# Optimization experiments

Measured on AMD Instinct MI355X. Metric: run time of the kernel, lower is better.

## Reference

```python
import jax, jax.numpy as jnp
import numpy as np

HIDDEN = 1024
Q_OUT = 2048
KV_OUT = 1024
HEAD_DIM = 128
N_Q = Q_OUT // HEAD_DIM      # 16
N_KV = KV_OUT // HEAD_DIM    # 8
EPS = 1e-6
ROPE_BASE = 10000.0


def _rms_norm(x, w, eps=EPS):
    # normalize over last dim (head_dim)
    ms = jnp.mean(x * x, axis=-1, keepdims=True)
    return x * jax.lax.rsqrt(ms + eps) * w


def _rope_cos_sin(t, dim=HEAD_DIM, base=ROPE_BASE):
    inv_freq = 1.0 / (base ** (jnp.arange(0, dim, 2, dtype=jnp.float32) / dim))
    pos = jnp.arange(t, dtype=jnp.float32)
    freqs = pos[:, None] * inv_freq[None, :]          # (T, D/2)
    emb = jnp.concatenate([freqs, freqs], axis=-1)    # (T, D)
    return jnp.cos(emb), jnp.sin(emb)


def _rotate_half(x):
    d = x.shape[-1] // 2
    return jnp.concatenate([-x[..., d:], x[..., :d]], axis=-1)


def setup_inputs() -> dict:
    key = jax.random.key(0)
    ks = jax.random.split(key, 7)
    def lin(k, fan_in, fan_out):
        # nn.Linear default init: U(-1/sqrt(fan_in), 1/sqrt(fan_in)); stored as (in, out) for x @ W
        bound = 1.0 / np.sqrt(fan_in)
        return jax.random.uniform(k, (fan_in, fan_out), jnp.float32, -bound, bound)
    return {
        "x": jax.random.normal(ks[0], (2, 2048, HIDDEN), jnp.float32),
        "Wq": lin(ks[1], HIDDEN, Q_OUT),
        "Wk": lin(ks[2], HIDDEN, KV_OUT),
        "Wv": lin(ks[3], HIDDEN, KV_OUT),
        "Wo": lin(ks[4], Q_OUT, HIDDEN),
        "q_norm_w": jnp.ones((HEAD_DIM,), jnp.float32),
        "k_norm_w": jnp.ones((HEAD_DIM,), jnp.float32),
    }


def reference(x, Wq, Wk, Wv, Wo, q_norm_w, k_norm_w):
    b, t, _ = x.shape
    # QKV projections, shaped to (B, H, T, D)
    q = (x @ Wq).reshape(b, t, N_Q, HEAD_DIM).transpose(0, 2, 1, 3)
    k = (x @ Wk).reshape(b, t, N_KV, HEAD_DIM).transpose(0, 2, 1, 3)
    v = (x @ Wv).reshape(b, t, N_KV, HEAD_DIM).transpose(0, 2, 1, 3)
    # per-head RMSNorm on q/k
    q = _rms_norm(q, q_norm_w)
    k = _rms_norm(k, k_norm_w)
    # RoPE (positions 0..T-1)
    cos, sin = _rope_cos_sin(t)                        # (T, D)
    cos = cos[None, None]; sin = sin[None, None]       # (1,1,T,D)
    q = q * cos + _rotate_half(q) * sin
    k = k * cos + _rotate_half(k) * sin
    # GQA: repeat_interleave kv heads to match q heads
    rep = N_Q // N_KV
    k_r = jnp.repeat(k, rep, axis=1)                   # (B, Hq, T, D)
    v_r = jnp.repeat(v, rep, axis=1)
    # causal attention
    scores = jnp.einsum('bhqd,bhkd->bhqk', q, k_r) / jnp.sqrt(jnp.asarray(HEAD_DIM, x.dtype))
    causal = jnp.triu(jnp.full((t, t), -jnp.inf, dtype=scores.dtype), k=1)[None, None]
    attn = jax.nn.softmax(scores + causal, axis=-1)
    out = jnp.einsum('bhqk,bhkd->bhqd', attn, v_r)     # (B, Hq, T, D)
    out = out.transpose(0, 2, 1, 3).reshape(b, t, Q_OUT)
    return out @ Wo
```

## Files before the change

kernel.cpp:

```cpp
#include <hip/hip_runtime.h>
#include <math.h>

typedef __attribute__((ext_vector_type(8))) short short8;
typedef __attribute__((ext_vector_type(4))) float f32x4;
typedef __attribute__((ext_vector_type(4))) unsigned int uint4v;

#define HIDDEN 1024
#define QOUT 2048
#define KVOUT 1024
#define HD 128
#define TSEQ 2048

__device__ __forceinline__ float bf2f(unsigned short h) {
    union { unsigned int u; float f; } x; x.u = ((unsigned int)h) << 16; return x.f;
}
__device__ __forceinline__ unsigned short f2bf(float f) {
    union { float f; unsigned int u; } x; x.f = f;
    unsigned int r = (x.u + 0x7fffu + ((x.u >> 16) & 1u)) >> 16;
    return (unsigned short)r;
}
__device__ __forceinline__ unsigned int cvtpk(float lo, float hi) {
    unsigned int r;
    asm("v_cvt_pk_bf16_f32 %0, %1, %2" : "=v"(r) : "v"(lo), "v"(hi));
    return r;
}

__device__ __forceinline__ void glds16(const unsigned short* g, unsigned short* l) {
    __builtin_amdgcn_global_load_lds(
        (const __attribute__((address_space(1))) unsigned int*)g,
        (__attribute__((address_space(3))) unsigned int*)l, 16, 0, 0);
}

__global__ __launch_bounds__(256) void prep(const float* __restrict__ x,
                                            const float* __restrict__ Wq,
                                            const float* __restrict__ Wk,
                                            const float* __restrict__ Wv,
                                            const float* __restrict__ Wo,
                                            unsigned short* __restrict__ xb,
                                            unsigned short* __restrict__ Wt,
                                            unsigned short* __restrict__ Wot) {
    int bid = blockIdx.x;
    int tid = threadIdx.x;
    if (bid < 4096) {
        int i = bid * 256 + tid;
        float4 v = *(const float4*)(x + (size_t)i * 4);
        unsigned short o[4] = {f2bf(v.x), f2bf(v.y), f2bf(v.z), f2bf(v.w)};
        *(unsigned long long*)(xb + (size_t)i * 4) = *(unsigned long long*)o;
        return;
    }
    bid -= 4096;
    const float* W; unsigned short* D; int K, N;
    if (bid < 512)       { W = Wq; D = Wt;                          K = 1024; N = 2048; }
    else if (bid < 768)  { bid -= 512;  W = Wk; D = Wt + (size_t)2048 * 1024; K = 1024; N = 1024; }
    else if (bid < 1024) { bid -= 768;  W = Wv; D = Wt + (size_t)3072 * 1024; K = 1024; N = 1024; }
    else                 { bid -= 1024; W = Wo; D = Wot;                      K = 2048; N = 1024; }
    __shared__ __attribute__((aligned(16))) unsigned short Ls[64 * 72];
    int ntiles = N >> 6;
    int kt = bid / ntiles, nt = bid - kt * ntiles;
    int k0 = kt * 64, n0 = nt * 64;
    for (int t = 0; t < 4; t++) {
        int idx = tid + t * 256;
        int r = idx >> 4, seg = idx & 15;
        float4 v = *(const float4*)(W + (size_t)(k0 + r) * N + n0 + seg * 4);
        int c = seg * 4;
        Ls[(c + 0) * 72 + r] = f2bf(v.x);
        Ls[(c + 1) * 72 + r] = f2bf(v.y);
        Ls[(c + 2) * 72 + r] = f2bf(v.z);
        Ls[(c + 3) * 72 + r] = f2bf(v.w);
    }
    __syncthreads();
    for (int t = 0; t < 2; t++) {
        int idx = tid + t * 256;
        int rr = idx >> 3, seg = idx & 7;
        uint4v v = *(const uint4v*)(Ls + rr * 72 + seg * 8);
        *(uint4v*)(D + (size_t)(n0 + rr) * K + k0 + seg * 8) = v;
    }
}

template <int OUT_BF16>
__global__ __launch_bounds__(256) void gemm_o(const unsigned short* __restrict__ A,
                                              const unsigned short* __restrict__ Bt,
                                              void* __restrict__ Cout,
                                              int M, int N, int K) {
    __shared__ __attribute__((aligned(16))) unsigned short As[2][128 * 64];
    __shared__ __attribute__((aligned(16))) unsigned short Bs[2][64 * 64];
    const int tid = threadIdx.x;
    const int lane = tid & 63;
    const int warp = tid >> 6;
    const int ln = lane & 15;
    const int quad = lane >> 4;
    const int m0 = blockIdx.y * 128;
    const int n0 = blockIdx.x * 64;

    const int srow = lane >> 3;
    const int schunk = (lane & 7) ^ srow;
    const unsigned short* Ag = A + (size_t)(m0 + warp * 32 + srow) * K + schunk * 8;
    const unsigned short* Bg = Bt + (size_t)(n0 + warp * 16 + srow) * K + schunk * 8;

    f32x4 acc[2][4];
#pragma unroll
    for (int i = 0; i < 2; i++)
#pragma unroll
        for (int j = 0; j < 4; j++) acc[i][j] = (f32x4){0.f, 0.f, 0.f, 0.f};

    auto stage = [&](int k0, int bi) {
#pragma unroll
        for (int g = 0; g < 4; g++)
            glds16(Ag + (size_t)(g * 8) * K + k0, As[bi] + (warp * 32 + g * 8) * 64);
#pragma unroll
        for (int g = 0; g < 2; g++)
            glds16(Bg + (size_t)(g * 8) * K + k0, Bs[bi] + (warp * 16 + g * 8) * 64);
    };

    const int KI = K >> 6;
    stage(0, 0);
    for (int it = 0; it < KI; it++) {
        __syncthreads();
        if (it + 1 < KI) stage((it + 1) << 6, (it + 1) & 1);
        const unsigned short* Ab = As[it & 1];
        const unsigned short* Bb = Bs[it & 1];
#pragma unroll
        for (int ks = 0; ks < 2; ks++) {
            const int rc = ((ks << 2) + quad) ^ (ln & 7);
            short8 af[2], bf[4];
#pragma unroll
            for (int mt = 0; mt < 2; mt++)
                af[mt] = *(const short8*)(Ab + (warp * 32 + mt * 16 + ln) * 64 + rc * 8);
#pragma unroll
            for (int nt = 0; nt < 4; nt++)
                bf[nt] = *(const short8*)(Bb + (nt * 16 + ln) * 64 + rc * 8);
#pragma unroll
            for (int mt = 0; mt < 2; mt++)
#pragma unroll
                for (int nt = 0; nt < 4; nt++)
                    acc[mt][nt] = __builtin_amdgcn_mfma_f32_16x16x32_bf16(bf[nt], af[mt], acc[mt][nt], 0, 0, 0);
        }
    }
#pragma unroll
    for (int mt = 0; mt < 2; mt++) {
        int row = m0 + warp * 32 + mt * 16 + ln;
#pragma unroll
        for (int nt = 0; nt < 4; nt++) {
            int colb = n0 + nt * 16 + quad * 4;
            if (OUT_BF16) {
                unsigned long long pk =
                    (unsigned long long)cvtpk(acc[mt][nt][0], acc[mt][nt][1]) |
                    ((unsigned long long)cvtpk(acc[mt][nt][2], acc[mt][nt][3]) << 32);
                *(unsigned long long*)((unsigned short*)Cout + (size_t)row * N + colb) = pk;
            } else {
                *(f32x4*)((float*)Cout + (size_t)row * N + colb) = acc[mt][nt];
            }
        }
    }
}

__global__ __launch_bounds__(256) void nrvt(const unsigned short* __restrict__ QKV,
                                            const float* __restrict__ qw,
                                            const float* __restrict__ kw,
                                            unsigned short* __restrict__ Q,
                                            unsigned short* __restrict__ Kb,
                                            unsigned short* __restrict__ Vt) {
    if (blockIdx.x < 12288) {
        const int tid = threadIdx.x;
        const int l5 = tid & 31;
        const int task = blockIdx.x * 8 + (tid >> 5);
        const int tok = task / 24;
        const int slot = task - tok * 24;
        const int b = tok >> 11, t = tok & 2047;
        const float* w;
        unsigned short* dst;
        int col0;
        float sc;
        if (slot < 16) {
            col0 = slot * HD;
            dst = Q + ((size_t)(b * 16 + slot) * TSEQ + t) * HD;
            w = qw;
            sc = 0.12750580997495268f;
        } else {
            int hk = slot - 16;
            col0 = QOUT + hk * HD;
            dst = Kb + ((size_t)(b * 8 + hk) * TSEQ + t) * HD;
            w = kw;
            sc = 1.0f;
        }
        const unsigned short* row = QKV + (size_t)tok * 4096 + col0;
        unsigned long long pkin = *(const unsigned long long*)(row + l5 * 4);
        unsigned short us[4];
        *(unsigned long long*)us = pkin;
        float e[4];
        float ss = 0.f;
#pragma unroll
        for (int k = 0; k < 4; k++) { e[k] = bf2f(us[k]); ss += e[k] * e[k]; }
#pragma unroll
        for (int off = 1; off < 32; off <<= 1) ss += __shfl_xor(ss, off);
        float rr = rsqrtf(ss * (1.0f / 128.0f) + 1e-6f);
        float4 wv = *(const float4*)(w + l5 * 4);
        float n[4] = { e[0] * rr * wv.x, e[1] * rr * wv.y, e[2] * rr * wv.z, e[3] * rr * wv.w };
        float np[4];
#pragma unroll
        for (int k = 0; k < 4; k++) np[k] = __shfl_xor(n[k], 16);
        const float tf = (float)t;
        const int fb = (l5 & 15) * 4;
        const bool hi = (l5 >= 16);
        unsigned short outs[4];
#pragma unroll
        for (int k = 0; k < 4; k++) {
            float invf = __builtin_exp2f(-(float)(fb + k) * 0.20762050593045951f);
            float sf, cf;
            __sincosf(tf * invf, &sf, &cf);
            float o = hi ? (n[k] * cf + np[k] * sf) : (n[k] * cf - np[k] * sf);
            outs[k] = f2bf(o * sc);
        }
        *(unsigned long long*)(dst + l5 * 4) = *(unsigned long long*)outs;
        return;
    }
    __shared__ __attribute__((aligned(16))) unsigned short Ls[128 * 72];
    int bid = blockIdx.x - 12288;
    int tt = bid & 31, hk = (bid >> 5) & 7, b = bid >> 8;
    int t0 = tt * 64;
    int tid = threadIdx.x;
    const unsigned short* base = QKV + (size_t)(b * 2048 + t0) * 4096 + 3072 + hk * 128;
    for (int i = 0; i < 4; i++) {
        int idx = tid + i * 256;
        int r = idx >> 4, seg = idx & 15;
        uint4v v = *(const uint4v*)(base + (size_t)r * 4096 + seg * 8);
        unsigned short* pv = (unsigned short*)&v;
        int d = seg * 8;
        for (int jj = 0; jj < 8; jj++) Ls[(d + jj) * 72 + r] = pv[jj];
    }
    __syncthreads();
    unsigned short* out = Vt + (size_t)(b * 8 + hk) * 128 * 2048;
    for (int i = 0; i < 4; i++) {
        int idx = tid + i * 256;
        int d = idx >> 3, seg = idx & 7;
        uint4v v = *(const uint4v*)(Ls + d * 72 + seg * 8);
        *(uint4v*)(out + (size_t)d * 2048 + t0 + seg * 8) = v;
    }
}

__global__ __launch_bounds__(512, 4) void attn(const unsigned short* __restrict__ Q,
                                               const unsigned short* __restrict__ Kg,
                                               const unsigned short* __restrict__ Vt,
                                               unsigned short* __restrict__ Og) {
    __shared__ __attribute__((aligned(16))) unsigned short Ks[2][64 * 128];
    __shared__ __attribute__((aligned(16))) unsigned short Vs[2][128 * 64];
    __shared__ __attribute__((aligned(16))) unsigned short Ps[8][8][16][8];
    const int p = blockIdx.x;
    const int bh = blockIdx.y;
    const int b = bh >> 4, h = bh & 15, hk = h >> 1;
    const int tid = threadIdx.x;
    const int w = tid >> 6, lane = tid & 63, ln = lane & 15, quad = lane >> 4;
    const int sg = w >> 2;
    const int wi = w & 3;
    const int tile = sg ? (31 - p) : p;
    const int jdiag = tile;
    const int qrow0 = tile * 64 + wi * 16;

    const unsigned short* Kbase = Kg + (size_t)(b * 8 + hk) * TSEQ * HD;
    const unsigned short* Vbase = Vt + (size_t)(b * 8 + hk) * HD * TSEQ;
    const unsigned short* Qh = Q + (size_t)(b * 16 + h) * TSEQ * HD;

    short8 qf[4];
#pragma unroll
    for (int kt = 0; kt < 4; kt++)
        qf[kt] = *(const short8*)(Qh + (size_t)(qrow0 + ln) * HD + kt * 32 + quad * 8);

    f32x4 o[8];
    f32x4 lac = (f32x4){0.f, 0.f, 0.f, 0.f};
#pragma unroll
    for (int ot = 0; ot < 8; ot++) o[ot] = (f32x4){0.f, 0.f, 0.f, 0.f};
    float m_ = -1e30f;

    const int kr = lane >> 4;
    const int kc = lane & 15;
    const int vr = lane >> 3;
    const int vc = lane & 7;

    auto stage_kv = [&](int jt, int bi) {
        const int j0s = jt * 64;
        unsigned short* KsB = Ks[bi];
        unsigned short* VsB = Vs[bi];
#pragma unroll
        for (int c = 0; c < 2; c++) {
            int row = w * 8 + c * 4 + kr;
            glds16(Kbase + (size_t)(j0s + row) * HD + ((kc ^ (row & 15)) * 8),
                   KsB + (w * 8 + c * 4) * 128);
        }
#pragma unroll
        for (int c = 0; c < 2; c++) {
            int d = w * 16 + c * 8 + vr;
            glds16(Vbase + (size_t)d * TSEQ + j0s + ((vc ^ (d & 7)) * 8),
                   VsB + (w * 16 + c * 8) * 64);
        }
    };

    short8 ones8;
#pragma unroll
    for (int i = 0; i < 8; i++) ones8[i] = (short)0x3F80;

    unsigned short* Pw = &Ps[w][0][0][0];
    const int nT = 32 - p;
    stage_kv(0, 0);
    for (int j = 0; j < nT; j++) {
        __syncthreads();
        if (j + 1 < nT) stage_kv(j + 1, (j + 1) & 1);
        const unsigned short* KsC = Ks[j & 1];
        const unsigned short* VsC = Vs[j & 1];
        const bool act = sg ? true : (j <= jdiag);
        if (act) {
            f32x4 s[4];
#pragma unroll
            for (int kb = 0; kb < 4; kb++) s[kb] = (f32x4){0.f, 0.f, 0.f, 0.f};
            __builtin_amdgcn_s_setprio(1);
#pragma unroll
            for (int kt = 0; kt < 4; kt++) {
                short8 kf[4];
#pragma unroll
                for (int kb = 0; kb < 4; kb++)
                    kf[kb] = *(const short8*)(KsC + (kb * 16 + ln) * 128 + (((kt * 4 + quad) ^ ln) * 8));
#pragma unroll
                for (int kb = 0; kb < 4; kb++)
                    s[kb] = __builtin_amdgcn_mfma_f32_16x16x32_bf16(kf[kb], qf[kt], s[kb], 0, 0, 0);
            }
            __builtin_amdgcn_s_setprio(0);
            float mk[4];
            if (j == jdiag) {
                const int qloc = wi * 16 + ln;
#pragma unroll
                for (int kb = 0; kb < 4; kb++) {
#pragma unroll
                    for (int r = 0; r < 4; r++) {
                        int kvloc = kb * 16 + quad * 4 + r;
                        if (kvloc > qloc) s[kb][r] = -1e30f;
                    }
                    mk[kb] = fmaxf(fmaxf(s[kb][0], s[kb][1]), fmaxf(s[kb][2], s[kb][3]));
                }
            } else {
#pragma unroll
                for (int kb = 0; kb < 4; kb++)
                    mk[kb] = fmaxf(fmaxf(s[kb][0], s[kb][1]), fmaxf(s[kb][2], s[kb][3]));
            }
            float mx = fmaxf(fmaxf(mk[0], mk[1]), fmaxf(mk[2], mk[3]));
            float mn = m_;
            bool needR = false;
            float alpha = 1.f;
            if (!__all(mx <= mn + 8.0f)) {
                mx = fmaxf(mx, __shfl_xor(mx, 16));
                mx = fmaxf(mx, __shfl_xor(mx, 32));
                mn = fmaxf(m_, mx);
                alpha = __builtin_exp2f(m_ - mn);
                m_ = mn;
                needR = true;
            }
#pragma unroll
            for (int kb = 0; kb < 4; kb++) {
                float p0 = __builtin_exp2f(s[kb][0] - mn);
                float p1 = __builtin_exp2f(s[kb][1] - mn);
                float p2 = __builtin_exp2f(s[kb][2] - mn);
                float p3 = __builtin_exp2f(s[kb][3] - mn);
                unsigned long long pk =
                    (unsigned long long)cvtpk(p0, p1) |
                    ((unsigned long long)cvtpk(p2, p3) << 32);
                *(unsigned long long*)(Pw + (2 * kb + (quad >> 1)) * 128 + ln * 8 + (quad & 1) * 4) = pk;
            }
            short8 pf0 = *(const short8*)(Pw + quad * 128 + ln * 8);
            short8 pf1 = *(const short8*)(Pw + (4 + quad) * 128 + ln * 8);
            if (needR) {
#pragma unroll
                for (int ot = 0; ot < 8; ot++)
#pragma unroll
                    for (int r = 0; r < 4; r++) o[ot][r] *= alpha;
#pragma unroll
                for (int r = 0; r < 4; r++) lac[r] *= alpha;
            }
            __builtin_amdgcn_s_setprio(1);
            lac = __builtin_amdgcn_mfma_f32_16x16x32_bf16(ones8, pf0, lac, 0, 0, 0);
            lac = __builtin_amdgcn_mfma_f32_16x16x32_bf16(ones8, pf1, lac, 0, 0, 0);
#pragma unroll
            for (int ot = 0; ot < 8; ot++) {
                short8 vf0 = *(const short8*)(VsC + (ot * 16 + ln) * 64 + ((quad ^ (ln & 7)) * 8));
                short8 vf1 = *(const short8*)(VsC + (ot * 16 + ln) * 64 + (((4 + quad) ^ (ln & 7)) * 8));
                o[ot] = __builtin_amdgcn_mfma_f32_16x16x32_bf16(vf0, pf0, o[ot], 0, 0, 0);
                o[ot] = __builtin_amdgcn_mfma_f32_16x16x32_bf16(vf1, pf1, o[ot], 0, 0, 0);
            }
            __builtin_amdgcn_s_setprio(0);
        }
    }
    float inv = 1.0f / lac[0];
    size_t rowoff = ((size_t)(b * TSEQ + qrow0 + ln)) * QOUT + h * 128 + quad * 4;
#pragma unroll
    for (int ot = 0; ot < 8; ot++) {
        unsigned long long pk =
            (unsigned long long)cvtpk(o[ot][0] * inv, o[ot][1] * inv) |
            ((unsigned long long)cvtpk(o[ot][2] * inv, o[ot][3] * inv) << 32);
        *(unsigned long long*)(Og + rowoff + ot * 16) = pk;
    }
}

extern "C" void kernel_launch(void* const* d_in, const int* in_sizes, int n_in,
                              void* d_out, int out_size, void* d_ws, size_t ws_size,
                              hipStream_t stream) {
    (void)in_sizes; (void)n_in; (void)out_size;
    const float* x  = (const float*)d_in[0];
    const float* Wq = (const float*)d_in[1];
    const float* Wk = (const float*)d_in[2];
    const float* Wv = (const float*)d_in[3];
    const float* Wo = (const float*)d_in[4];
    const float* qw = (const float*)d_in[5];
    const float* kw = (const float*)d_in[6];

    char* ws = (char*)d_ws;
    const size_t MB = 1024 * 1024;
    unsigned short* Wt   = (unsigned short*)(ws);
    unsigned short* Wot  = (unsigned short*)(ws + 8 * MB);
    unsigned short* QKVb = (unsigned short*)(ws + 12 * MB);
    unsigned short* xb   = (unsigned short*)(ws + 44 * MB);
    unsigned short* Qb   = (unsigned short*)(ws + 52 * MB);
    unsigned short* Kb   = (unsigned short*)(ws + 68 * MB);
    unsigned short* Vtb  = (unsigned short*)(ws + 76 * MB);
    unsigned short* Ob   = (unsigned short*)(ws + 84 * MB);
    if (ws_size < 100 * MB) return;

    prep<<<dim3(5632), 256, 0, stream>>>(x, Wq, Wk, Wv, Wo, xb, Wt, Wot);
    gemm_o<1><<<dim3(64, 32), 256, 0, stream>>>(xb, Wt, QKVb, 4096, 4096, 1024);
    nrvt<<<dim3(12800), 256, 0, stream>>>(QKVb, qw, kw, Qb, Kb, Vtb);
    attn<<<dim3(16, 32), 512, 0, stream>>>(Qb, Kb, Vtb, Ob);
    gemm_o<0><<<dim3(16, 32), 256, 0, stream>>>(Ob, Wot, (float*)d_out, 4096, 1024, 2048);
}
```

Baseline: 254.4 us.

## Add 256x256 8-wave QKV GEMM, permlane P-repack, and balanced attention tile order

Replaces the QKV projection GEMM with a new 512-thread kernel using 256x256 tiles, a double-buffered LDS pipeline and interleaved barriers. The aim is more operand reuse and better overlap of global loads with MFMA work. In attention, the P matrix is now repacked into MFMA operand layout with permlane16/32 swaps instead of an LDS round trip. Causal tiles are also remapped so short and long blocks alternate. Together these target LDS traffic, GEMM memory bandwidth and load imbalance, at the cost of more registers and a more intricate fragment layout that must stay correct.

```diff
diff --git a/kernel.cpp b/kernel.cpp
--- a/kernel.cpp
+++ b/kernel.cpp
@@ -23,6 +23,12 @@
     unsigned int r;
     asm("v_cvt_pk_bf16_f32 %0, %1, %2" : "=v"(r) : "v"(lo), "v"(hi));
     return r;
+}
+__device__ __forceinline__ void pl32(unsigned int& a, unsigned int& b) {
+    asm("v_permlane32_swap_b32 %0, %1" : "+v"(a), "+v"(b));
+}
+__device__ __forceinline__ void pl16(unsigned int& a, unsigned int& b) {
+    asm("v_permlane16_swap_b32 %0, %1" : "+v"(a), "+v"(b));
 }
 
 __device__ __forceinline__ void glds16(const unsigned short* g, unsigned short* l) {
@@ -75,6 +81,140 @@
         uint4v v = *(const uint4v*)(Ls + rr * 72 + seg * 8);
         *(uint4v*)(D + (size_t)(n0 + rr) * K + k0 + seg * 8) = v;
     }
+}
+
+__global__ __launch_bounds__(512, 2) void gemm8(const unsigned short* __restrict__ A,
+                                                const unsigned short* __restrict__ Bt,
+                                                unsigned short* __restrict__ Cout,
+                                                int M, int N, int K) {
+    (void)M;
+    __shared__ __attribute__((aligned(16))) unsigned short L[2][4][128 * 64];
+    const int tid = threadIdx.x;
+    const int lane = tid & 63;
+    const int w = tid >> 6;
+    const int ln = lane & 15;
+    const int quad = lane >> 4;
+    const int wm2 = w >> 2;
+    const int wn4 = w & 3;
+    const int m0 = blockIdx.y * 256;
+    const int n0 = blockIdx.x * 256;
+
+    const int srow8 = lane >> 3;
+    const int schunk = (lane & 7) ^ srow8;
+    const int KS = K >> 6;
+    const int NJ = K >> 7;
+
+    f32x4 acc[2][2][4][2];
+#pragma unroll
+    for (int a = 0; a < 2; a++)
+#pragma unroll
+        for (int b = 0; b < 2; b++)
+#pragma unroll
+            for (int c = 0; c < 4; c++)
+#pragma unroll
+                for (int d = 0; d < 2; d++) acc[a][b][c][d] = (f32x4){0.f, 0.f, 0.f, 0.f};
+
+    auto issue = [&](int ks_, int half) {
+        if (ks_ >= KS) return;
+        const unsigned short* src = (half < 2) ? A : Bt;
+        const int rbase = ((half < 2) ? m0 : n0) + (half & 1) * 128;
+        unsigned short* dst = &L[ks_ & 1][half][0];
+#pragma unroll
+        for (int g = 0; g < 2; g++) {
+            glds16(src + (size_t)(rbase + w * 16 + g * 8 + srow8) * K + ks_ * 64 + schunk * 8,
+                   dst + (w * 16 + g * 8) * 64);
+        }
+    };
+
+    short8 af[4][2];
+    short8 bfr[2][2][2];
+
+#define RD_A(LB, RH)                                                                     \
+    _Pragma("unroll") for (int rt = 0; rt < 4; rt++)                                     \
+        _Pragma("unroll") for (int ks = 0; ks < 2; ks++)                                 \
+            af[rt][ks] = *(const short8*)((LB) + ((RH)*64 + rt * 16 + ln) * 64 +         \
+                                          ((((ks << 2) + quad) ^ (ln & 7)) * 8));
+
+#define RD_B(LB, CH)                                                                     \
+    _Pragma("unroll") for (int ct = 0; ct < 2; ct++)                                     \
+        _Pragma("unroll") for (int ks = 0; ks < 2; ks++)                                 \
+            bfr[CH][ct][ks] = *(const short8*)((LB) + ((wn4 & 1) * 64 + (CH)*32 +        \
+                                               ct * 16 + ln) * 64 +                      \
+                                               ((((ks << 2) + quad) ^ (ln & 7)) * 8));
+
+#define MMA_Q(RH, CH)                                                                    \
+    __builtin_amdgcn_s_setprio(1);                                                       \
+    _Pragma("unroll") for (int ks = 0; ks < 2; ks++)                                     \
+        _Pragma("unroll") for (int rt = 0; rt < 4; rt++)                                 \
+            _Pragma("unroll") for (int ct = 0; ct < 2; ct++)                             \
+                acc[RH][CH][rt][ct] = __builtin_amdgcn_mfma_f32_16x16x32_bf16(           \
+                    bfr[CH][ct][ks], af[rt][ks], acc[RH][CH][rt][ct], 0, 0, 0);          \
+    __builtin_amdgcn_s_setprio(0);
+
+#define BAR() __builtin_amdgcn_s_barrier()
+
+    issue(0, 0); issue(0, 1); issue(0, 2); issue(0, 3);
+    issue(1, 2); issue(1, 3);
+    asm volatile("s_waitcnt vmcnt(4)" ::: "memory");
+    BAR();
+
+    for (int j = 0; j < NJ; j++) {
+        const bool last = (j == NJ - 1);
+        const unsigned short* A0 = &L[0][wm2][0];
+        const unsigned short* B0 = &L[0][2 + (wn4 >> 1)][0];
+        const unsigned short* A1 = &L[1][wm2][0];
+        const unsigned short* B1 = &L[1][2 + (wn4 >> 1)][0];
+        const int k1 = 2 * j + 1, k2 = 2 * j + 2, k3 = 2 * j + 3;
+        RD_A(A0, 0); RD_B(B0, 0);
+        issue(k1, 0);
+        BAR(); MMA_Q(0, 0); BAR();
+        RD_B(B0, 1);
+        issue(k1, 1);
+        BAR(); MMA_Q(0, 1); BAR();
+        RD_A(A0, 1);
+        issue(k2, 2);
+        BAR(); MMA_Q(1, 1); BAR();
+        issue(k2, 3);
+        BAR(); MMA_Q(1, 0);
+        if (last) { asm volatile("s_waitcnt vmcnt(0)" ::: "memory"); }
+        else      { asm volatile("s_waitcnt vmcnt(4)" ::: "memory"); }
+        BAR();
+        RD_A(A1, 0); RD_B(B1, 0);
+        issue(k2, 0);
+        BAR(); MMA_Q(0, 0); BAR();
+        RD_B(B1, 1);
+        issue(k2, 1);
+        BAR(); MMA_Q(0, 1); BAR();
+        RD_A(A1, 1);
+        issue(k3, 2);
+        BAR(); MMA_Q(1, 1); BAR();
+        issue(k3, 3);
+        BAR(); MMA_Q(1, 0);
+        if (!last) { asm volatile("s_waitcnt vmcnt(4)" ::: "memory"); }
+        BAR();
+    }
+
+#pragma unroll
+    for (int rh = 0; rh < 2; rh++)
+#pragma unroll
+        for (int rt = 0; rt < 4; rt++) {
+            int row = m0 + wm2 * 128 + rh * 64 + rt * 16 + ln;
+#pragma unroll
+            for (int ch = 0; ch < 2; ch++)
+#pragma unroll
+                for (int ct = 0; ct < 2; ct++) {
+                    int colb = n0 + wn4 * 64 + ch * 32 + ct * 16 + quad * 4;
+                    f32x4 v = acc[rh][ch][rt][ct];
+                    unsigned long long pk =
+                        (unsigned long long)cvtpk(v[0], v[1]) |
+                        ((unsigned long long)cvtpk(v[2], v[3]) << 32);
+                    *(unsigned long long*)(Cout + (size_t)row * N + colb) = pk;
+                }
+        }
+#undef RD_A
+#undef RD_B
+#undef MMA_Q
+#undef BAR
 }
 
 template <int OUT_BF16>
@@ -244,8 +384,8 @@
                                                unsigned short* __restrict__ Og) {
     __shared__ __attribute__((aligned(16))) unsigned short Ks[2][64 * 128];
     __shared__ __attribute__((aligned(16))) unsigned short Vs[2][128 * 64];
-    __shared__ __attribute__((aligned(16))) unsigned short Ps[8][8][16][8];
-    const int p = blockIdx.x;
+    const int px = blockIdx.x;
+    const int p = (px & 1) ? (15 - (px >> 1)) : (px >> 1);
     const int bh = blockIdx.y;
     const int b = bh >> 4, h = bh & 15, hk = h >> 1;
     const int tid = threadIdx.x;
@@ -298,7 +438,6 @@
 #pragma unroll
     for (int i = 0; i < 8; i++) ones8[i] = (short)0x3F80;
 
-    unsigned short* Pw = &Ps[w][0][0][0];
     const int nT = 32 - p;
     stage_kv(0, 0);
     for (int j = 0; j < nT; j++) {
@@ -352,19 +491,25 @@
                 m_ = mn;
                 needR = true;
             }
+            unsigned int u[8];
 #pragma unroll
             for (int kb = 0; kb < 4; kb++) {
                 float p0 = __builtin_exp2f(s[kb][0] - mn);
                 float p1 = __builtin_exp2f(s[kb][1] - mn);
                 float p2 = __builtin_exp2f(s[kb][2] - mn);
                 float p3 = __builtin_exp2f(s[kb][3] - mn);
-                unsigned long long pk =
-                    (unsigned long long)cvtpk(p0, p1) |
-                    ((unsigned long long)cvtpk(p2, p3) << 32);
-                *(unsigned long long*)(Pw + (2 * kb + (quad >> 1)) * 128 + ln * 8 + (quad & 1) * 4) = pk;
-            }
-            short8 pf0 = *(const short8*)(Pw + quad * 128 + ln * 8);
-            short8 pf1 = *(const short8*)(Pw + (4 + quad) * 128 + ln * 8);
+                u[kb * 2 + 0] = cvtpk(p0, p1);
+                u[kb * 2 + 1] = cvtpk(p2, p3);
+            }
+            pl32(u[0], u[2]); pl16(u[0], u[2]);
+            pl32(u[1], u[3]); pl16(u[1], u[3]);
+            pl32(u[4], u[6]); pl16(u[4], u[6]);
+            pl32(u[5], u[7]); pl16(u[5], u[7]);
+            union { unsigned int uu[4]; short8 s8; } P0, P1;
+            P0.uu[0] = u[0]; P0.uu[1] = u[1]; P0.uu[2] = u[2]; P0.uu[3] = u[3];
+            P1.uu[0] = u[4]; P1.uu[1] = u[5]; P1.uu[2] = u[6]; P1.uu[3] = u[7];
+            short8 pf0 = P0.s8;
+            short8 pf1 = P1.s8;
             if (needR) {
 #pragma unroll
                 for (int ot = 0; ot < 8; ot++)
@@ -422,7 +567,7 @@
     if (ws_size < 100 * MB) return;
 
     prep<<<dim3(5632), 256, 0, stream>>>(x, Wq, Wk, Wv, Wo, xb, Wt, Wot);
-    gemm_o<1><<<dim3(64, 32), 256, 0, stream>>>(xb, Wt, QKVb, 4096, 4096, 1024);
+    gemm8<<<dim3(16, 16), 512, 0, stream>>>(xb, Wt, QKVb, 4096, 4096, 1024);
     nrvt<<<dim3(12800), 256, 0, stream>>>(QKVb, qw, kw, Qb, Kb, Vtb);
     attn<<<dim3(16, 32), 512, 0, stream>>>(Qb, Kb, Vtb, Ob);
     gemm_o<0><<<dim3(16, 32), 256, 0, stream>>>(Ob, Wot, (float*)d_out, 4096, 1024, 2048);
```

Measured after the change: 247.7 us. 1.03x faster.
